# Kernel tuning notes

Hardware: AMD Instinct MI355X
Metric: run time of the kernel (lower is better)

The kernel has to match this reference:

```python
import jax, jax.numpy as jnp
import numpy as np

DIM, EXP = 512, 16
INTERNAL = DIM * EXP  # 8192
BATCH, SEQ = 2, 2048


def setup_inputs() -> dict:
    key = jax.random.key(0)
    ks = jax.random.split(key, 8)
    s = 0.02
    return {
        "x": jax.random.normal(ks[0], (BATCH, SEQ, DIM), jnp.float32),
        "W_dt_w": jax.random.normal(ks[1], (INTERNAL, DIM), jnp.float32) * s,
        "W_dt_b": jnp.zeros((INTERNAL,), jnp.float32),
        "W_B_w": jax.random.normal(ks[2], (INTERNAL, DIM), jnp.float32) * s,
        "W_B_b": jnp.zeros((INTERNAL,), jnp.float32),
        "W_C_w": jax.random.normal(ks[3], (INTERNAL, DIM), jnp.float32) * s,
        "W_C_b": jnp.zeros((INTERNAL,), jnp.float32),
        "W_V_w": jax.random.normal(ks[4], (INTERNAL, DIM), jnp.float32) * s,
        "W_V_b": jnp.zeros((INTERNAL,), jnp.float32),
        # A_log = -rand(internal): negative for stability, as in torch init
        "A_log": -jax.random.uniform(ks[5], (INTERNAL,), jnp.float32),
        "W_out_w": jax.random.normal(ks[6], (DIM, INTERNAL), jnp.float32) * s,
        "W_out_b": jnp.zeros((DIM,), jnp.float32),
    }


def _scan_combine(c1, c2):
    # semi-separable recurrence h_t = a_t * h_{t-1} + b_t, as associative op
    a1, b1 = c1
    a2, b2 = c2
    return a2 * a1, a2 * b1 + b2


def reference(x, W_dt_w, W_dt_b, W_B_w, W_B_b, W_C_w, W_C_b,
              W_V_w, W_V_b, A_log, W_out_w, W_out_b):
    # Featurizer10: discretized SSM features. Shapes: x [b,s,d] -> [b,s,n]
    dt = jax.nn.softplus(jnp.einsum('bsd,nd->bsn', x, W_dt_w) + W_dt_b)
    A_bar = jnp.exp(dt * A_log)                                  # S: [b,s,n]
    B_bar = dt * (jnp.einsum('bsd,nd->bsn', x, W_B_w) + W_B_b)   # B: [b,s,n]
    C = jnp.einsum('bsd,nd->bsn', x, W_C_w) + W_C_b              # C: [b,s,n]
    V = jnp.einsum('bsd,nd->bsn', x, W_V_w) + W_V_b              # V: [b,s,n]
    # Token mixing: h_t = A_bar_t * h_{t-1} + B_bar_t * V_t (parallel scan)
    u = B_bar * V
    _, h = jax.lax.associative_scan(_scan_combine, (A_bar, u), axis=1)
    y = C * h                                                    # [b,s,n]
    # Output projection back to model dim
    return jnp.einsum('bsn,dn->bsd', y, W_out_w) + W_out_b
```

## Files before the change

### kernel.cpp

```cpp
#include <hip/hip_runtime.h>

#define DIMK 512
#define NCH  8192
#define NCAT 32768
#define MTOT 4096
#define SEQL 2048
#define KS   4

typedef __attribute__((ext_vector_type(8))) short bf16x8;
typedef __attribute__((ext_vector_type(4))) float f32x4;
typedef unsigned int uint32;

__device__ __forceinline__ unsigned short f2bf(float f) {
  unsigned int u = __float_as_uint(f);
  u += 0x7fffu + ((u >> 16) & 1u);
  return (unsigned short)(u >> 16);
}
__device__ __forceinline__ float bf2f(unsigned short v) {
  return __uint_as_float(((unsigned int)v) << 16);
}

struct CvtArgs {
  const float* src[6];
  unsigned short* dst[6];
  int cum[7];
};
__global__ __launch_bounds__(256) void cvt_all_kernel(CvtArgs a, int tot) {
  const int stride = gridDim.x * 256;
  for (int i = blockIdx.x * 256 + threadIdx.x; i < tot; i += stride) {
    int s = 0;
    while (i >= a.cum[s + 1]) ++s;
    const int j = i - a.cum[s];
    const float4* sp = reinterpret_cast<const float4*>(a.src[s]);
    float4 v0 = sp[2 * j], v1 = sp[2 * j + 1];
    union { unsigned short us[8]; uint4 v; } o;
    o.us[0] = f2bf(v0.x); o.us[1] = f2bf(v0.y); o.us[2] = f2bf(v0.z); o.us[3] = f2bf(v0.w);
    o.us[4] = f2bf(v1.x); o.us[5] = f2bf(v1.y); o.us[6] = f2bf(v1.z); o.us[7] = f2bf(v1.w);
    int dj = j;
    if (s >= 1 && s <= 4) {
      const int row = j >> 6, k8 = j & 63, p = s - 1;
      const int ncat = (row >> 4) * 64 + (p << 4) + (row & 15);
      dj = ncat * 64 + k8;
    }
    reinterpret_cast<uint4*>(a.dst[s])[dj] = o.v;
  }
}

__global__ __launch_bounds__(512) void proj_kernel(
    const unsigned short* __restrict__ xb,
    const unsigned short* __restrict__ wcat,
    const float* __restrict__ b_dt, const float* __restrict__ b_B,
    const float* __restrict__ b_C, const float* __restrict__ b_V,
    const float* __restrict__ A_log,
    uint32* __restrict__ au,
    unsigned short* __restrict__ c_out)
{
  __shared__ __align__(16) unsigned short lds_all[65536];
  unsigned short* ldsA = lds_all;
  unsigned short* ldsB = lds_all + 32768;

  const int tid = threadIdx.x;
  const int lane = tid & 63;
  const int wave = tid >> 6;
  const int wr = wave >> 2;
  const int wc = wave & 3;
  const int l15 = lane & 15, l4 = lane >> 4;
  const int bx = blockIdx.x;
  const int m0 = blockIdx.y * 256;

  auto stage_half = [&](int bsel, int kt, int kind) {
    const int k0 = kt * 64;
    #pragma unroll
    for (int i = 0; i < 2; ++i) {
      const int s = i * 512 + tid;
      const int rl = s >> 3, q = s & 7;
      const int row = (kind & 1) * 128 + rl;
      const int ksrc = q ^ (row & 7);
      if (kind < 2) {
        const unsigned short* g = xb + (size_t)(m0 + row) * DIMK + k0 + ksrc * 8;
        __builtin_amdgcn_global_load_lds(
            (const __attribute__((address_space(1))) void*)g,
            (__attribute__((address_space(3))) void*)&ldsA[bsel * 16384 + row * 64 + q * 8],
            16, 0, 0);
      } else {
        const unsigned short* g = wcat + (size_t)(bx * 256 + row) * DIMK + k0 + ksrc * 8;
        __builtin_amdgcn_global_load_lds(
            (const __attribute__((address_space(1))) void*)g,
            (__attribute__((address_space(3))) void*)&ldsB[bsel * 16384 + row * 64 + q * 8],
            16, 0, 0);
      }
    }
  };

  f32x4 acc[8][4];
  #pragma unroll
  for (int fm = 0; fm < 8; ++fm)
    #pragma unroll
    for (int fn = 0; fn < 4; ++fn) acc[fm][fn] = (f32x4){0.f, 0.f, 0.f, 0.f};

  stage_half(0, 0, 0); stage_half(0, 0, 1); stage_half(0, 0, 2); stage_half(0, 0, 3);

  constexpr int NT = DIMK / 64;
  #pragma unroll 1
  for (int t = 0; t < NT; ++t) {
    const int bsel = t & 1;
    asm volatile("s_waitcnt vmcnt(0)" ::: "memory");
    __builtin_amdgcn_s_barrier();
    bf16x8 bfr[4];
    #pragma unroll
    for (int ph = 0; ph < 4; ++ph) {
      const int ks = ph >> 1, fmg = ph & 1;
      const int qk = ks * 4 + l4;
      bf16x8 af[4];
      #pragma unroll
      for (int i = 0; i < 4; ++i) {
        const int r = wr * 128 + (fmg * 4 + i) * 16 + l15;
        af[i] = *reinterpret_cast<const bf16x8*>(
            &ldsA[bsel * 16384 + r * 64 + (qk ^ (r & 7)) * 8]);
      }
      if (fmg == 0) {
        #pragma unroll
        for (int fn = 0; fn < 4; ++fn) {
          const int rb = wc * 64 + fn * 16 + l15;
          bfr[fn] = *reinterpret_cast<const bf16x8*>(
              &ldsB[bsel * 16384 + rb * 64 + (qk ^ (rb & 7)) * 8]);
        }
      }
      if (t + 1 < NT && ph < 2) {
        stage_half(bsel ^ 1, t + 1, ph * 2 + 0);
        stage_half(bsel ^ 1, t + 1, ph * 2 + 1);
      }
      __builtin_amdgcn_s_barrier();
      asm volatile("s_waitcnt lgkmcnt(0)" ::: "memory");
      __builtin_amdgcn_sched_barrier(0);
      __builtin_amdgcn_s_setprio(1);
      #pragma unroll
      for (int i = 0; i < 4; ++i)
        #pragma unroll
        for (int fn = 0; fn < 4; ++fn)
          acc[fmg * 4 + i][fn] = __builtin_amdgcn_mfma_f32_16x16x32_bf16(
              af[i], bfr[fn], acc[fmg * 4 + i][fn], 0, 0, 0);
      __builtin_amdgcn_s_setprio(0);
      __builtin_amdgcn_s_barrier();
    }
  }

  const int ch = bx * 64 + wc * 16 + l15;
  const float vbdt = b_dt[ch], vbB = b_B[ch], vbC = b_C[ch], vbV = b_V[ch];
  const float al = A_log[ch];
  #pragma unroll
  for (int fm = 0; fm < 8; ++fm) {
    const int mb = m0 + wr * 128 + fm * 16 + l4 * 4;
    #pragma unroll
    for (int r = 0; r < 4; ++r) {
      const size_t off = (size_t)(mb + r) * NCH + ch;
      const float zdt = acc[fm][0][r] + vbdt;
      const float zB  = acc[fm][1][r] + vbB;
      const float zC  = acc[fm][2][r] + vbC;
      const float zV  = acc[fm][3][r] + vbV;
      const float dt = (zdt > 15.f) ? zdt : __logf(1.f + __expf(zdt));
      au[off] = ((uint32)f2bf(dt * al) << 16) | (uint32)f2bf(dt * zB * zV);
      c_out[off] = f2bf(zC);
    }
  }
}

#define SCH 16
#define CSTEPS 128
__global__ __launch_bounds__(1024) void scan_kernel(
    const uint32* __restrict__ au,
    unsigned short* cy)
{
  __shared__ float Ap[SCH][64], He[SCH][64], H0[SCH][64];
  const int lane = threadIdx.x & 63;
  const int w = threadIdx.x >> 6;
  const int c = blockIdx.x * 64 + lane;
  const size_t base = (size_t)blockIdx.y * SEQL * NCH + (size_t)(w * CSTEPS) * NCH + c;

  {
    const uint32* ap = au + base;
    float h = 0.f, vsum = 0.f;
    #pragma unroll 1
    for (int s = 0; s < CSTEPS; s += 8) {
      uint32 wv[8];
      #pragma unroll
      for (int i = 0; i < 8; ++i) wv[i] = ap[(size_t)(s + i) * NCH];
      #pragma unroll
      for (int i = 0; i < 8; ++i) {
        const float av = bf2f((unsigned short)(wv[i] >> 16));
        const float uv = bf2f((unsigned short)(wv[i] & 0xffff));
        vsum += av;
        h = fmaf(__expf(av), h, uv);
      }
    }
    Ap[w][lane] = __expf(vsum);
    He[w][lane] = h;
  }
  __syncthreads();
  if (w == 0) {
    float run = 0.f;
    #pragma unroll
    for (int jj = 0; jj < SCH; ++jj) {
      H0[jj][lane] = run;
      run = fmaf(Ap[jj][lane], run, He[jj][lane]);
    }
  }
  __syncthreads();
  {
    const uint32* ap = au + base;
    unsigned short* cp = cy + base;
    float h = H0[w][lane];
    #pragma unroll 1
    for (int s = 0; s < CSTEPS; s += 8) {
      uint32 wv[8];
      float cv[8];
      #pragma unroll
      for (int i = 0; i < 8; ++i) {
        wv[i] = ap[(size_t)(s + i) * NCH];
        cv[i] = bf2f(cp[(size_t)(s + i) * NCH]);
      }
      #pragma unroll
      for (int i = 0; i < 8; ++i) {
        const float av = bf2f((unsigned short)(wv[i] >> 16));
        const float uv = bf2f((unsigned short)(wv[i] & 0xffff));
        h = fmaf(__expf(av), h, uv);
        cv[i] *= h;
      }
      #pragma unroll
      for (int i = 0; i < 8; ++i) cp[(size_t)(s + i) * NCH] = f2bf(cv[i]);
    }
  }
}

__device__ __forceinline__ int swz(int row, int q) { return q ^ ((row >> 2) & 3); }

#define OLDS_A 4096
#define OLDS_B 2048
#define OLDS   (OLDS_A + OLDS_B)
__global__ __launch_bounds__(256) void outproj_kernel(
    const unsigned short* __restrict__ yb,
    const unsigned short* __restrict__ wout,
    float* __restrict__ partial)
{
  __shared__ __align__(16) unsigned short lds[2][OLDS];
  const int tid = threadIdx.x;
  const int lane = tid & 63;
  const int wave = tid >> 6;
  const int wr = wave >> 1, wc = wave & 1;
  const int m0 = blockIdx.x * 128;
  const int d0 = blockIdx.y * 64;
  const int kbase = blockIdx.z * (NCH / KS);

  auto stage = [&](int buf, int kt) {
    const int k0 = kbase + kt * 32;
    #pragma unroll
    for (int i = 0; i < 2; ++i) {
      int c = i * 256 + tid;
      int row = c >> 2, q = c & 3;
      const unsigned short* g = yb + (size_t)(m0 + row) * NCH + k0 + swz(row, q) * 8;
      __builtin_amdgcn_global_load_lds(
          (const __attribute__((address_space(1))) void*)g,
          (__attribute__((address_space(3))) void*)&lds[buf][c * 8], 16, 0, 0);
    }
    {
      int row = tid >> 2, q = tid & 3;
      const unsigned short* g = wout + (size_t)(d0 + row) * NCH + k0 + swz(row, q) * 8;
      __builtin_amdgcn_global_load_lds(
          (const __attribute__((address_space(1))) void*)g,
          (__attribute__((address_space(3))) void*)&lds[buf][OLDS_A + tid * 8], 16, 0, 0);
    }
  };

  f32x4 acc[4][2];
  #pragma unroll
  for (int fm = 0; fm < 4; ++fm)
    #pragma unroll
    for (int fn = 0; fn < 2; ++fn) acc[fm][fn] = (f32x4){0.f, 0.f, 0.f, 0.f};

  stage(0, 0);
  constexpr int NKT = (NCH / KS) / 32;
  #pragma unroll 1
  for (int kt = 0; kt < NKT; ++kt) {
    const int buf = kt & 1;
    if (kt + 1 < NKT) {
      stage(buf ^ 1, kt + 1);
      asm volatile("s_waitcnt vmcnt(3)" ::: "memory");
    } else {
      asm volatile("s_waitcnt vmcnt(0)" ::: "memory");
    }
    __builtin_amdgcn_s_barrier();

    const int qq = lane >> 4;
    bf16x8 af[4], bfr[2];
    #pragma unroll
    for (int fm = 0; fm < 4; ++fm) {
      const int r = wr * 64 + fm * 16 + (lane & 15);
      af[fm] = *reinterpret_cast<const bf16x8*>(&lds[buf][r * 32 + swz(r, qq) * 8]);
    }
    #pragma unroll
    for (int fn = 0; fn < 2; ++fn) {
      const int r = wc * 32 + fn * 16 + (lane & 15);
      bfr[fn] = *reinterpret_cast<const bf16x8*>(
          &lds[buf][OLDS_A + r * 32 + swz(r, qq) * 8]);
    }
    __builtin_amdgcn_s_setprio(1);
    #pragma unroll
    for (int fm = 0; fm < 4; ++fm)
      #pragma unroll
      for (int fn = 0; fn < 2; ++fn)
        acc[fm][fn] = __builtin_amdgcn_mfma_f32_16x16x32_bf16(
            af[fm], bfr[fn], acc[fm][fn], 0, 0, 0);
    __builtin_amdgcn_s_setprio(0);
    asm volatile("s_waitcnt lgkmcnt(0)" ::: "memory");
    __builtin_amdgcn_s_barrier();
  }

  float* pout = partial + (size_t)blockIdx.z * MTOT * DIMK;
  #pragma unroll
  for (int fn = 0; fn < 2; ++fn) {
    const int d = d0 + wc * 32 + fn * 16 + (lane & 15);
    #pragma unroll
    for (int fm = 0; fm < 4; ++fm) {
      const int mbase = m0 + wr * 64 + fm * 16 + (lane >> 4) * 4;
      #pragma unroll
      for (int r = 0; r < 4; ++r)
        pout[(size_t)(mbase + r) * DIMK + d] = acc[fm][fn][r];
    }
  }
}

__global__ __launch_bounds__(256) void reduce_kernel(
    const float* __restrict__ p, const float* __restrict__ bias,
    float* __restrict__ out)
{
  const int i = blockIdx.x * 256 + threadIdx.x;
  const float4* p4 = reinterpret_cast<const float4*>(p);
  float4 s = p4[i];
  #pragma unroll
  for (int k = 1; k < KS; ++k) {
    float4 t = p4[(size_t)k * (MTOT * DIMK / 4) + i];
    s.x += t.x; s.y += t.y; s.z += t.z; s.w += t.w;
  }
  const float4 b = reinterpret_cast<const float4*>(bias)[i & 127];
  s.x += b.x; s.y += b.y; s.z += b.z; s.w += b.w;
  reinterpret_cast<float4*>(out)[i] = s;
}

extern "C" void kernel_launch(void* const* d_in, const int* in_sizes, int n_in,
                              void* d_out, int out_size, void* d_ws, size_t ws_size,
                              hipStream_t stream) {
  const float* x    = (const float*)d_in[0];
  const float* Wdt  = (const float*)d_in[1];
  const float* bdt  = (const float*)d_in[2];
  const float* WB   = (const float*)d_in[3];
  const float* bB   = (const float*)d_in[4];
  const float* WC   = (const float*)d_in[5];
  const float* bC   = (const float*)d_in[6];
  const float* WV   = (const float*)d_in[7];
  const float* bV   = (const float*)d_in[8];
  const float* Alog = (const float*)d_in[9];
  const float* Wout = (const float*)d_in[10];
  const float* bout = (const float*)d_in[11];
  float* out = (float*)d_out;

  char* ws = (char*)d_ws;
  unsigned short* woutb = (unsigned short*)(ws);
  unsigned short* xb    = (unsigned short*)(ws + 8388608);
  unsigned short* wcat  = (unsigned short*)(ws + 12582912);
  char* dyn = ws + 46137344;
  uint32*         au  = (uint32*)(dyn);
  unsigned short* cy  = (unsigned short*)(dyn + (size_t)MTOT * NCH * 4);
  float* partial = (float*)au;

  CvtArgs ca;
  ca.src[0] = x;    ca.dst[0] = xb;
  ca.src[1] = Wdt;  ca.dst[1] = wcat;
  ca.src[2] = WB;   ca.dst[2] = wcat;
  ca.src[3] = WC;   ca.dst[3] = wcat;
  ca.src[4] = WV;   ca.dst[4] = wcat;
  ca.src[5] = Wout; ca.dst[5] = woutb;
  ca.cum[0] = 0;        ca.cum[1] = 262144;  ca.cum[2] = 786432;
  ca.cum[3] = 1310720;  ca.cum[4] = 1835008; ca.cum[5] = 2359296;
  ca.cum[6] = 2883584;
  cvt_all_kernel<<<2048, 256, 0, stream>>>(ca, 2883584);

  proj_kernel<<<dim3(NCAT / 256, MTOT / 256), 512, 0, stream>>>(
      xb, wcat, bdt, bB, bC, bV, Alog, au, cy);
  scan_kernel<<<dim3(NCH / 64, 2), 1024, 0, stream>>>(au, cy);
  outproj_kernel<<<dim3(MTOT / 128, DIMK / 64, KS), 256, 0, stream>>>(
      cy, woutb, partial);
  reduce_kernel<<<MTOT * DIMK / 4 / 256, 256, 0, stream>>>(partial, bout, out);
}
```

Before: 414.8 us.

## Triple-buffer projection and output GEMMs and halve the projection M tile

Both GEMM kernels move from double to triple buffering in LDS. Loads for tile t+2 are issued while tile t is computed, and the per-phase barriers are dropped, leaving one barrier per k-step. The projection kernel also shrinks its M tile from 256 to 128 rows, which doubles the grid and halves the accumulator registers, so per-block reuse of the weight tiles goes down. LDS use in the projection kernel grows to about 144 KB, which limits each CU to one block.

```diff
diff --git a/kernel.cpp b/kernel.cpp
--- a/kernel.cpp
+++ b/kernel.cpp
@@ -55,9 +55,9 @@
     uint32* __restrict__ au,
     unsigned short* __restrict__ c_out)
 {
-  __shared__ __align__(16) unsigned short lds_all[65536];
+  __shared__ __align__(16) unsigned short lds_all[73728];
   unsigned short* ldsA = lds_all;
-  unsigned short* ldsB = lds_all + 32768;
+  unsigned short* ldsB = lds_all + 24576;
 
   const int tid = threadIdx.x;
   const int lane = tid & 63;
@@ -66,71 +66,74 @@
   const int wc = wave & 3;
   const int l15 = lane & 15, l4 = lane >> 4;
   const int bx = blockIdx.x;
-  const int m0 = blockIdx.y * 256;
-
-  auto stage_half = [&](int bsel, int kt, int kind) {
+  const int m0 = blockIdx.y * 128;
+
+  auto stageA = [&](int bsel, int kt) {
     const int k0 = kt * 64;
     #pragma unroll
     for (int i = 0; i < 2; ++i) {
       const int s = i * 512 + tid;
-      const int rl = s >> 3, q = s & 7;
-      const int row = (kind & 1) * 128 + rl;
+      const int row = s >> 3, q = s & 7;
       const int ksrc = q ^ (row & 7);
-      if (kind < 2) {
-        const unsigned short* g = xb + (size_t)(m0 + row) * DIMK + k0 + ksrc * 8;
-        __builtin_amdgcn_global_load_lds(
-            (const __attribute__((address_space(1))) void*)g,
-            (__attribute__((address_space(3))) void*)&ldsA[bsel * 16384 + row * 64 + q * 8],
-            16, 0, 0);
-      } else {
-        const unsigned short* g = wcat + (size_t)(bx * 256 + row) * DIMK + k0 + ksrc * 8;
-        __builtin_amdgcn_global_load_lds(
-            (const __attribute__((address_space(1))) void*)g,
-            (__attribute__((address_space(3))) void*)&ldsB[bsel * 16384 + row * 64 + q * 8],
-            16, 0, 0);
-      }
+      const unsigned short* g = xb + (size_t)(m0 + row) * DIMK + k0 + ksrc * 8;
+      __builtin_amdgcn_global_load_lds(
+          (const __attribute__((address_space(1))) void*)g,
+          (__attribute__((address_space(3))) void*)&ldsA[bsel * 8192 + row * 64 + q * 8],
+          16, 0, 0);
     }
   };
-
-  f32x4 acc[8][4];
-  #pragma unroll
-  for (int fm = 0; fm < 8; ++fm)
+  auto stageB = [&](int bsel, int kt, int half) {
+    const int k0 = kt * 64;
+    #pragma unroll
+    for (int i = 0; i < 2; ++i) {
+      const int s = half * 1024 + i * 512 + tid;
+      const int row = s >> 3, q = s & 7;
+      const int ksrc = q ^ (row & 7);
+      const unsigned short* g = wcat + (size_t)(bx * 256 + row) * DIMK + k0 + ksrc * 8;
+      __builtin_amdgcn_global_load_lds(
+          (const __attribute__((address_space(1))) void*)g,
+          (__attribute__((address_space(3))) void*)&ldsB[bsel * 16384 + row * 64 + q * 8],
+          16, 0, 0);
+    }
+  };
+
+  f32x4 acc[4][4];
+  #pragma unroll
+  for (int fm = 0; fm < 4; ++fm)
     #pragma unroll
     for (int fn = 0; fn < 4; ++fn) acc[fm][fn] = (f32x4){0.f, 0.f, 0.f, 0.f};
 
-  stage_half(0, 0, 0); stage_half(0, 0, 1); stage_half(0, 0, 2); stage_half(0, 0, 3);
+  stageA(0, 0); stageB(0, 0, 0); stageB(0, 0, 1);
+  stageA(1, 1); stageB(1, 1, 0); stageB(1, 1, 1);
 
   constexpr int NT = DIMK / 64;
   #pragma unroll 1
   for (int t = 0; t < NT; ++t) {
-    const int bsel = t & 1;
-    asm volatile("s_waitcnt vmcnt(0)" ::: "memory");
+    const int bsel = t % 3;
+    if (t < NT - 1) asm volatile("s_waitcnt vmcnt(6)" ::: "memory");
+    else            asm volatile("s_waitcnt vmcnt(0)" ::: "memory");
     __builtin_amdgcn_s_barrier();
-    bf16x8 bfr[4];
-    #pragma unroll
-    for (int ph = 0; ph < 4; ++ph) {
-      const int ks = ph >> 1, fmg = ph & 1;
+
+    #pragma unroll
+    for (int ks = 0; ks < 2; ++ks) {
       const int qk = ks * 4 + l4;
-      bf16x8 af[4];
+      bf16x8 af[4], bf[4];
       #pragma unroll
       for (int i = 0; i < 4; ++i) {
-        const int r = wr * 128 + (fmg * 4 + i) * 16 + l15;
+        const int r = wr * 64 + i * 16 + l15;
         af[i] = *reinterpret_cast<const bf16x8*>(
-            &ldsA[bsel * 16384 + r * 64 + (qk ^ (r & 7)) * 8]);
-      }
-      if (fmg == 0) {
-        #pragma unroll
-        for (int fn = 0; fn < 4; ++fn) {
-          const int rb = wc * 64 + fn * 16 + l15;
-          bfr[fn] = *reinterpret_cast<const bf16x8*>(
-              &ldsB[bsel * 16384 + rb * 64 + (qk ^ (rb & 7)) * 8]);
-        }
-      }
-      if (t + 1 < NT && ph < 2) {
-        stage_half(bsel ^ 1, t + 1, ph * 2 + 0);
-        stage_half(bsel ^ 1, t + 1, ph * 2 + 1);
-      }
-      __builtin_amdgcn_s_barrier();
+            &ldsA[bsel * 8192 + r * 64 + ((qk ^ (r & 7))) * 8]);
+      }
+      #pragma unroll
+      for (int fn = 0; fn < 4; ++fn) {
+        const int rb = wc * 64 + fn * 16 + l15;
+        bf[fn] = *reinterpret_cast<const bf16x8*>(
+            &ldsB[bsel * 16384 + rb * 64 + ((qk ^ (rb & 7))) * 8]);
+      }
+      if (t + 2 < NT) {
+        if (ks == 0) { stageA((t + 2) % 3, t + 2); stageB((t + 2) % 3, t + 2, 0); }
+        else         { stageB((t + 2) % 3, t + 2, 1); }
+      }
       asm volatile("s_waitcnt lgkmcnt(0)" ::: "memory");
       __builtin_amdgcn_sched_barrier(0);
       __builtin_amdgcn_s_setprio(1);
@@ -138,10 +141,9 @@
       for (int i = 0; i < 4; ++i)
         #pragma unroll
         for (int fn = 0; fn < 4; ++fn)
-          acc[fmg * 4 + i][fn] = __builtin_amdgcn_mfma_f32_16x16x32_bf16(
-              af[i], bfr[fn], acc[fmg * 4 + i][fn], 0, 0, 0);
+          acc[i][fn] = __builtin_amdgcn_mfma_f32_16x16x32_bf16(
+              af[i], bf[fn], acc[i][fn], 0, 0, 0);
       __builtin_amdgcn_s_setprio(0);
-      __builtin_amdgcn_s_barrier();
     }
   }
 
@@ -149,8 +151,8 @@
   const float vbdt = b_dt[ch], vbB = b_B[ch], vbC = b_C[ch], vbV = b_V[ch];
   const float al = A_log[ch];
   #pragma unroll
-  for (int fm = 0; fm < 8; ++fm) {
-    const int mb = m0 + wr * 128 + fm * 16 + l4 * 4;
+  for (int fm = 0; fm < 4; ++fm) {
+    const int mb = m0 + wr * 64 + fm * 16 + l4 * 4;
     #pragma unroll
     for (int r = 0; r < 4; ++r) {
       const size_t off = (size_t)(mb + r) * NCH + ch;
@@ -242,7 +244,7 @@
     const unsigned short* __restrict__ wout,
     float* __restrict__ partial)
 {
-  __shared__ __align__(16) unsigned short lds[2][OLDS];
+  __shared__ __align__(16) unsigned short lds[3][OLDS];
   const int tid = threadIdx.x;
   const int lane = tid & 63;
   const int wave = tid >> 6;
@@ -278,16 +280,13 @@
     for (int fn = 0; fn < 2; ++fn) acc[fm][fn] = (f32x4){0.f, 0.f, 0.f, 0.f};
 
   stage(0, 0);
+  stage(1, 1);
   constexpr int NKT = (NCH / KS) / 32;
   #pragma unroll 1
   for (int kt = 0; kt < NKT; ++kt) {
-    const int buf = kt & 1;
-    if (kt + 1 < NKT) {
-      stage(buf ^ 1, kt + 1);
-      asm volatile("s_waitcnt vmcnt(3)" ::: "memory");
-    } else {
-      asm volatile("s_waitcnt vmcnt(0)" ::: "memory");
-    }
+    const int buf = kt % 3;
+    if (kt < NKT - 1) asm volatile("s_waitcnt vmcnt(3)" ::: "memory");
+    else              asm volatile("s_waitcnt vmcnt(0)" ::: "memory");
     __builtin_amdgcn_s_barrier();
 
     const int qq = lane >> 4;
@@ -303,6 +302,9 @@
       bfr[fn] = *reinterpret_cast<const bf16x8*>(
           &lds[buf][OLDS_A + r * 32 + swz(r, qq) * 8]);
     }
+    if (kt + 2 < NKT) stage((kt + 2) % 3, kt + 2);
+    asm volatile("s_waitcnt lgkmcnt(0)" ::: "memory");
+    __builtin_amdgcn_sched_barrier(0);
     __builtin_amdgcn_s_setprio(1);
     #pragma unroll
     for (int fm = 0; fm < 4; ++fm)
@@ -311,8 +313,6 @@
         acc[fm][fn] = __builtin_amdgcn_mfma_f32_16x16x32_bf16(
             af[fm], bfr[fn], acc[fm][fn], 0, 0, 0);
     __builtin_amdgcn_s_setprio(0);
-    asm volatile("s_waitcnt lgkmcnt(0)" ::: "memory");
-    __builtin_amdgcn_s_barrier();
   }
 
   float* pout = partial + (size_t)blockIdx.z * MTOT * DIMK;
@@ -384,7 +384,7 @@
   ca.cum[6] = 2883584;
   cvt_all_kernel<<<2048, 256, 0, stream>>>(ca, 2883584);
 
-  proj_kernel<<<dim3(NCAT / 256, MTOT / 256), 512, 0, stream>>>(
+  proj_kernel<<<dim3(NCAT / 256, MTOT / 128), 512, 0, stream>>>(
       xb, wcat, bdt, bB, bC, bV, Alog, au, cy);
   scan_kernel<<<dim3(NCH / 64, 2), 1024, 0, stream>>>(au, cy);
   outproj_kernel<<<dim3(MTOT / 128, DIMK / 64, KS), 256, 0, stream>>>(
```

Measured after the change: 443.0 us. 1.07x slower.

## Fuse per-chunk scan summaries into projection epilogue, drop scan's first pass

Applied to the files above, without the earlier changes.

The projection epilogue now computes, per channel, the (A-product, h-end) summary of each 256-row block using in-register combination, wave shuffles and an LDS merge between the two wave rows, and writes them to a scratch buffer placed in the output array. The scan kernel no longer re-reads the au tensor to build chunk carries. Each wave prefixes the summaries of earlier chunks and runs a single pass over 256 steps, so one full read of au is removed. This adds epilogue work to the GEMM, and it halves the scan's parallelism, with 512 threads and longer serial chains.

```diff
diff --git a/kernel.cpp b/kernel.cpp
--- a/kernel.cpp
+++ b/kernel.cpp
@@ -53,7 +53,8 @@
     const float* __restrict__ b_C, const float* __restrict__ b_V,
     const float* __restrict__ A_log,
     uint32* __restrict__ au,
-    unsigned short* __restrict__ c_out)
+    unsigned short* __restrict__ c_out,
+    float2* __restrict__ summ)
 {
   __shared__ __align__(16) unsigned short lds_all[65536];
   unsigned short* ldsA = lds_all;
@@ -148,9 +149,11 @@
   const int ch = bx * 64 + wc * 16 + l15;
   const float vbdt = b_dt[ch], vbB = b_B[ch], vbC = b_C[ch], vbV = b_V[ch];
   const float al = A_log[ch];
+  float Aw = 1.f, Bw = 0.f;
   #pragma unroll
   for (int fm = 0; fm < 8; ++fm) {
     const int mb = m0 + wr * 128 + fm * 16 + l4 * 4;
+    float Ar = 1.f, Br = 0.f;
     #pragma unroll
     for (int r = 0; r < 4; ++r) {
       const size_t off = (size_t)(mb + r) * NCH + ch;
@@ -159,76 +162,69 @@
       const float zC  = acc[fm][2][r] + vbC;
       const float zV  = acc[fm][3][r] + vbV;
       const float dt = (zdt > 15.f) ? zdt : __logf(1.f + __expf(zdt));
-      au[off] = ((uint32)f2bf(dt * al) << 16) | (uint32)f2bf(dt * zB * zV);
+      const unsigned short vl_us = f2bf(dt * al);
+      const unsigned short u_us  = f2bf(dt * zB * zV);
+      au[off] = ((uint32)vl_us << 16) | (uint32)u_us;
       c_out[off] = f2bf(zC);
-    }
-  }
-}
-
-#define SCH 16
-#define CSTEPS 128
-__global__ __launch_bounds__(1024) void scan_kernel(
+      const float a = __expf(bf2f(vl_us));
+      Br = fmaf(a, Br, bf2f(u_us));
+      Ar *= a;
+    }
+    {
+      float Ao = __shfl_xor(Ar, 16), Bo = __shfl_xor(Br, 16);
+      Br = (lane & 16) ? fmaf(Ar, Bo, Br) : fmaf(Ao, Br, Bo);
+      Ar *= Ao;
+      Ao = __shfl_xor(Ar, 32); Bo = __shfl_xor(Br, 32);
+      Br = (lane & 32) ? fmaf(Ar, Bo, Br) : fmaf(Ao, Br, Bo);
+      Ar *= Ao;
+    }
+    Bw = fmaf(Ar, Bw, Br);
+    Aw *= Ar;
+  }
+  float2* sm = reinterpret_cast<float2*>(lds_all);
+  if (wr == 0 && l4 == 0) sm[wc * 16 + l15] = make_float2(Aw, Bw);
+  __syncthreads();
+  if (wr == 1 && l4 == 0) {
+    const float2 lo = sm[wc * 16 + l15];
+    summ[(size_t)blockIdx.y * NCH + ch] = make_float2(Aw * lo.x, fmaf(Aw, lo.y, Bw));
+  }
+}
+
+__global__ __launch_bounds__(512) void scan_kernel(
     const uint32* __restrict__ au,
+    const float2* __restrict__ summ,
     unsigned short* cy)
 {
-  __shared__ float Ap[SCH][64], He[SCH][64], H0[SCH][64];
   const int lane = threadIdx.x & 63;
   const int w = threadIdx.x >> 6;
   const int c = blockIdx.x * 64 + lane;
-  const size_t base = (size_t)blockIdx.y * SEQL * NCH + (size_t)(w * CSTEPS) * NCH + c;
-
-  {
-    const uint32* ap = au + base;
-    float h = 0.f, vsum = 0.f;
-    #pragma unroll 1
-    for (int s = 0; s < CSTEPS; s += 8) {
-      uint32 wv[8];
-      #pragma unroll
-      for (int i = 0; i < 8; ++i) wv[i] = ap[(size_t)(s + i) * NCH];
-      #pragma unroll
-      for (int i = 0; i < 8; ++i) {
-        const float av = bf2f((unsigned short)(wv[i] >> 16));
-        const float uv = bf2f((unsigned short)(wv[i] & 0xffff));
-        vsum += av;
-        h = fmaf(__expf(av), h, uv);
-      }
-    }
-    Ap[w][lane] = __expf(vsum);
-    He[w][lane] = h;
-  }
-  __syncthreads();
-  if (w == 0) {
-    float run = 0.f;
-    #pragma unroll
-    for (int jj = 0; jj < SCH; ++jj) {
-      H0[jj][lane] = run;
-      run = fmaf(Ap[jj][lane], run, He[jj][lane]);
-    }
-  }
-  __syncthreads();
-  {
-    const uint32* ap = au + base;
-    unsigned short* cp = cy + base;
-    float h = H0[w][lane];
-    #pragma unroll 1
-    for (int s = 0; s < CSTEPS; s += 8) {
-      uint32 wv[8];
-      float cv[8];
-      #pragma unroll
-      for (int i = 0; i < 8; ++i) {
-        wv[i] = ap[(size_t)(s + i) * NCH];
-        cv[i] = bf2f(cp[(size_t)(s + i) * NCH]);
-      }
-      #pragma unroll
-      for (int i = 0; i < 8; ++i) {
-        const float av = bf2f((unsigned short)(wv[i] >> 16));
-        const float uv = bf2f((unsigned short)(wv[i] & 0xffff));
-        h = fmaf(__expf(av), h, uv);
-        cv[i] *= h;
-      }
-      #pragma unroll
-      for (int i = 0; i < 8; ++i) cp[(size_t)(s + i) * NCH] = f2bf(cv[i]);
-    }
+  const int batch = blockIdx.y;
+  float h = 0.f;
+  for (int j = 0; j < w; ++j) {
+    const float2 s = summ[(size_t)(batch * 8 + j) * NCH + c];
+    h = fmaf(s.x, h, s.y);
+  }
+  const size_t base = (size_t)batch * SEQL * NCH + (size_t)(w * 256) * NCH + c;
+  const uint32* ap = au + base;
+  unsigned short* cp = cy + base;
+  #pragma unroll 1
+  for (int s = 0; s < 256; s += 8) {
+    uint32 wv[8];
+    float cv[8];
+    #pragma unroll
+    for (int i = 0; i < 8; ++i) {
+      wv[i] = ap[(size_t)(s + i) * NCH];
+      cv[i] = bf2f(cp[(size_t)(s + i) * NCH]);
+    }
+    #pragma unroll
+    for (int i = 0; i < 8; ++i) {
+      const float av = bf2f((unsigned short)(wv[i] >> 16));
+      const float uv = bf2f((unsigned short)(wv[i] & 0xffff));
+      h = fmaf(__expf(av), h, uv);
+      cv[i] *= h;
+    }
+    #pragma unroll
+    for (int i = 0; i < 8; ++i) cp[(size_t)(s + i) * NCH] = f2bf(cv[i]);
   }
 }
 
@@ -371,6 +367,7 @@
   uint32*         au  = (uint32*)(dyn);
   unsigned short* cy  = (unsigned short*)(dyn + (size_t)MTOT * NCH * 4);
   float* partial = (float*)au;
+  float2* summ = (float2*)d_out;
 
   CvtArgs ca;
   ca.src[0] = x;    ca.dst[0] = xb;
@@ -385,8 +382,8 @@
   cvt_all_kernel<<<2048, 256, 0, stream>>>(ca, 2883584);
 
   proj_kernel<<<dim3(NCAT / 256, MTOT / 256), 512, 0, stream>>>(
-      xb, wcat, bdt, bB, bC, bV, Alog, au, cy);
-  scan_kernel<<<dim3(NCH / 64, 2), 1024, 0, stream>>>(au, cy);
+      xb, wcat, bdt, bB, bC, bV, Alog, au, cy, summ);
+  scan_kernel<<<dim3(NCH / 64, 2), 512, 0, stream>>>(au, summ, cy);
   outproj_kernel<<<dim3(MTOT / 128, DIMK / 64, KS), 256, 0, stream>>>(
       cy, woutb, partial);
   reduce_kernel<<<MTOT * DIMK / 4 / 256, 256, 0, stream>>>(partial, bout, out);
```

Measured after the change: 425.4 us. 1.03x slower.
